# Performance work log

Measured on AMD Instinct MI355X. Metric: run time of the kernel, lower is better.

Reference implementation:

```python
import jax, jax.numpy as jnp
import numpy as np

EPS = 1e-6
DIM, HEADS, HEAD_DIM, FFN = 1024, 16, 64, 4096
B, S = 2, 2048


def layer_norm(x, g, b):
    m = jnp.mean(x, axis=-1, keepdims=True)
    v = jnp.mean(jnp.square(x - m), axis=-1, keepdims=True)
    return (x - m) * jax.lax.rsqrt(v + EPS) * g + b


def apply_rope(x, cos, sin):
    # x: (b, h, s, d); cos/sin: (s, d) broadcast over b, h
    x1, x2 = jnp.split(x, 2, axis=-1)
    rot = jnp.concatenate([-x2, x1], axis=-1)
    return x * cos + rot * sin


def setup_inputs() -> dict:
    key = jax.random.key(0)
    ks = jax.random.split(key, 24)
    sc_in = 1.0 / np.sqrt(DIM)
    sc_ffn = 1.0 / np.sqrt(FFN)
    inp = {
        "x": jax.random.normal(ks[0], (B, S, DIM), jnp.float32),
        "rope_cos": jax.random.uniform(ks[1], (S, HEAD_DIM), jnp.float32),
        "rope_sin": jax.random.uniform(ks[2], (S, HEAD_DIM), jnp.float32),
        "w_qkv": jax.random.normal(ks[3], (3 * DIM, DIM), jnp.float32) * sc_in,
        "b_qkv": jnp.zeros((3 * DIM,), jnp.float32),
        "w_out": jax.random.normal(ks[4], (DIM, DIM), jnp.float32) * sc_in,
        "b_out": jnp.zeros((DIM,), jnp.float32),
        "qn_g": jnp.ones((DIM,), jnp.float32),
        "qn_b": jnp.zeros((DIM,), jnp.float32),
        "kn_g": jnp.ones((DIM,), jnp.float32),
        "kn_b": jnp.zeros((DIM,), jnp.float32),
        "ln1_g": jnp.ones((DIM,), jnp.float32),
        "ln1_b": jnp.zeros((DIM,), jnp.float32),
        "ln2_g": jnp.ones((DIM,), jnp.float32),
        "ln2_b": jnp.zeros((DIM,), jnp.float32),
        "w1": jax.random.normal(ks[5], (FFN, DIM), jnp.float32) * sc_in,
        "b1": jnp.zeros((FFN,), jnp.float32),
        "w2": jax.random.normal(ks[6], (DIM, FFN), jnp.float32) * sc_ffn,
        "b2": jnp.zeros((DIM,), jnp.float32),
        "w3": jax.random.normal(ks[7], (FFN, DIM), jnp.float32) * sc_in,
        "b3": jnp.zeros((FFN,), jnp.float32),
    }
    return inp


def reference(x, rope_cos, rope_sin, w_qkv, b_qkv, w_out, b_out,
              qn_g, qn_b, kn_g, kn_b, ln1_g, ln1_b, ln2_g, ln2_b,
              w1, b1, w2, b2, w3, b3):
    bs, s, d = x.shape
    # --- pre-norm self-attention ---
    h = layer_norm(x, ln1_g, ln1_b)
    qkv = h @ w_qkv.T + b_qkv                      # (b, s, 3d)
    q, k, v = jnp.split(qkv, 3, axis=-1)
    q = layer_norm(q, qn_g, qn_b)                  # QK-norm over full dim
    k = layer_norm(k, kn_g, kn_b)
    # (b, s, d) -> (b, h, s, hd)
    q = q.reshape(bs, s, HEADS, HEAD_DIM).transpose(0, 2, 1, 3)
    k = k.reshape(bs, s, HEADS, HEAD_DIM).transpose(0, 2, 1, 3)
    v = v.reshape(bs, s, HEADS, HEAD_DIM).transpose(0, 2, 1, 3)
    q = apply_rope(q, rope_cos, rope_sin)
    k = apply_rope(k, rope_cos, rope_sin)
    scale = 1.0 / np.sqrt(HEAD_DIM)
    scores = jnp.einsum('bhqd,bhkd->bhqk', q, k) * scale
    probs = jax.nn.softmax(scores, axis=-1)
    attn = jnp.einsum('bhqk,bhkd->bhqd', probs, v)
    attn = attn.transpose(0, 2, 1, 3).reshape(bs, s, d)
    x = x + (attn @ w_out.T + b_out)
    # --- pre-norm SwiGLU FFN ---
    h2 = layer_norm(x, ln2_g, ln2_b)
    ffn = (jax.nn.silu(h2 @ w1.T + b1) * (h2 @ w3.T + b3)) @ w2.T + b2
    return x + ffn
```

## Files before the change

### kernel.cpp

```cpp
#include <hip/hip_runtime.h>
#include <hip/hip_bf16.h>


typedef __bf16 bf16_t;
typedef bf16_t bf16x8 __attribute__((ext_vector_type(8)));
typedef bf16_t bf16x4 __attribute__((ext_vector_type(4)));
typedef float  f32x4  __attribute__((ext_vector_type(4)));
typedef float  f32x16 __attribute__((ext_vector_type(16)));

#define DIM   1024
#define HEADS 16
#define HD    64
#define FFND  4096
#define NB    2
#define SEQ   2048
#define NTOK  (NB * SEQ)

#define GLOAD16(gp, lp) __builtin_amdgcn_global_load_lds( \
    (const __attribute__((address_space(1))) void*)(gp),  \
    (__attribute__((address_space(3))) void*)(lp), 16, 0, 0)

#define CVTPK(lo, hi_) ({ unsigned r_;                                        \
  asm("v_cvt_pk_bf16_f32 %0, %1, %2" : "=v"(r_) : "v"(lo), "v"(hi_)); r_; })
#define PLSWAP(a, b) asm("v_permlane32_swap_b32 %0, %1" : "+v"(a), "+v"(b))

#define F2B_S0 786432
#define F2B_S1 262144
#define F2B_S2 1048576
#define F2B_S3 1048576
#define F2B_S4 1048576
#define F2B_C1 (F2B_S0)
#define F2B_C2 (F2B_C1 + F2B_S1)
#define F2B_C3 (F2B_C2 + F2B_S2)
#define F2B_C4 (F2B_C3 + F2B_S3)
#define F2B_N  (F2B_C4 + F2B_S4)

__global__ void f2bf_all_kernel(const float* __restrict__ s0, const float* __restrict__ s1,
                                const float* __restrict__ s2, const float* __restrict__ s3,
                                const float* __restrict__ s4,
                                bf16_t* __restrict__ d0, bf16_t* __restrict__ d1,
                                bf16_t* __restrict__ d2, bf16_t* __restrict__ d3,
                                bf16_t* __restrict__ d4) {
  int idx = blockIdx.x * blockDim.x + threadIdx.x;
  int stride = gridDim.x * blockDim.x;
  for (; idx < F2B_N; idx += stride) {
    const float* src; bf16_t* dst; int i;
    if (idx < F2B_C1)      { src = s0; dst = d0; i = idx; }
    else if (idx < F2B_C2) { src = s1; dst = d1; i = idx - F2B_C1; }
    else if (idx < F2B_C3) { src = s2; dst = d2; i = idx - F2B_C2; }
    else if (idx < F2B_C4) { src = s3; dst = d3; i = idx - F2B_C3; }
    else                   { src = s4; dst = d4; i = idx - F2B_C4; }
    float4 v = reinterpret_cast<const float4*>(src)[i];
    bf16x4 o;
    o[0] = (bf16_t)v.x; o[1] = (bf16_t)v.y; o[2] = (bf16_t)v.z; o[3] = (bf16_t)v.w;
    reinterpret_cast<bf16x4*>(dst)[i] = o;
  }
}

__global__ __launch_bounds__(256) void ln_kernel(
    const float* __restrict__ x, const float* __restrict__ g,
    const float* __restrict__ b, bf16_t* __restrict__ out) {
  int t = blockIdx.x;
  int i = threadIdx.x;
  float4 v = reinterpret_cast<const float4*>(x + (size_t)t * DIM)[i];
  float s  = v.x + v.y + v.z + v.w;
  float s2 = v.x * v.x + v.y * v.y + v.z * v.z + v.w * v.w;
#pragma unroll
  for (int off = 32; off > 0; off >>= 1) {
    s  += __shfl_down(s, off, 64);
    s2 += __shfl_down(s2, off, 64);
  }
  __shared__ float red[2][4];
  int wid = i >> 6, lane = i & 63;
  if (lane == 0) { red[0][wid] = s; red[1][wid] = s2; }
  __syncthreads();
  float S  = red[0][0] + red[0][1] + red[0][2] + red[0][3];
  float S2 = red[1][0] + red[1][1] + red[1][2] + red[1][3];
  float mean = S * (1.0f / DIM);
  float var  = S2 * (1.0f / DIM) - mean * mean;
  float r = rsqrtf(var + 1e-6f);
  float vv[4] = {v.x, v.y, v.z, v.w};
  bf16x4 o;
#pragma unroll
  for (int j = 0; j < 4; ++j) {
    int d = i * 4 + j;
    o[j] = (bf16_t)((vv[j] - mean) * r * g[d] + b[d]);
  }
  *reinterpret_cast<bf16x4*>(out + (size_t)t * DIM + i * 4) = o;
}

template <int OUT_MODE>
__global__ __launch_bounds__(512, 2) void gemm256(
    const bf16_t* __restrict__ A, const bf16_t* __restrict__ B,
    const float* __restrict__ bias, const bf16_t* __restrict__ comp,
    void* __restrict__ Cout, int M, int N, int Kfull, int Klen) {
  __shared__ __align__(16) bf16_t Al[2][256][64];
  __shared__ __align__(16) bf16_t Bl[2][256][64];
  const int nTn = N >> 8;
  const int nwg = gridDim.x;
  const int bid = blockIdx.x;
  const int swz = ((nwg & 7) == 0) ? ((bid & 7) * (nwg >> 3) + (bid >> 3)) : bid;
  const int bm = swz / nTn, bn = swz % nTn;
  const int k0base = blockIdx.z * Klen;
  const int NT = Klen >> 6;
  const int tid = threadIdx.x, wid = tid >> 6, lane = tid & 63;
  const int wm = wid >> 2, wn = wid & 3;
  const int lr = lane & 15, lg = lane >> 4;
  const int strow = wid * 8 + (lane >> 3);
  const int stg   = ((lane & 7) ^ ((lane >> 3) & 7)) << 3;
  const bf16_t* Abase = A + (size_t)(bm * 256 + strow) * Kfull + k0base + stg;
  const bf16_t* Bbase = B + (size_t)(bn * 256 + strow) * Kfull + k0base + stg;

#define STAGE_A(buf, half, c, t)                                              \
  GLOAD16(Abase + (size_t)((half) * 128 + (c) * 64) * Kfull + (t) * 64,       \
          &Al[buf][(half) * 128 + (c) * 64 + wid * 8][0])
#define STAGE_B(buf, half, c, t)                                              \
  GLOAD16(Bbase + (size_t)((half) * 128 + (c) * 64) * Kfull + (t) * 64,       \
          &Bl[buf][(half) * 128 + (c) * 64 + wid * 8][0])

  f32x4 acc[8][4] = {};
  STAGE_A(0, 0, 0, 0); STAGE_A(0, 0, 1, 0); STAGE_A(0, 1, 0, 0); STAGE_A(0, 1, 1, 0);
  STAGE_B(0, 0, 0, 0); STAGE_B(0, 0, 1, 0); STAGE_B(0, 1, 0, 0); STAGE_B(0, 1, 1, 0);

  for (int t = 0; t < NT; ++t) {
    const int cur = t & 1, nxt = cur ^ 1;
    const bool pf = (t + 1 < NT);
    if (pf) {
      STAGE_A(nxt, 0, 0, t + 1); STAGE_A(nxt, 0, 1, t + 1);
      STAGE_A(nxt, 1, 0, t + 1); STAGE_A(nxt, 1, 1, t + 1);
      asm volatile("s_waitcnt vmcnt(4)");
    } else {
      asm volatile("s_waitcnt vmcnt(0)");
    }
    __builtin_amdgcn_sched_barrier(0);
    __builtin_amdgcn_s_barrier();
    __builtin_amdgcn_sched_barrier(0);
    bf16x8 bfr[4][2], af[2][2];
#pragma unroll
    for (int nf = 0; nf < 4; ++nf)
#pragma unroll
      for (int ks = 0; ks < 2; ++ks) {
        const int row = wn * 64 + nf * 16 + lr;
        const int g = ((ks * 4 + lg) ^ (lane & 7)) << 3;
        bfr[nf][ks] = *reinterpret_cast<const bf16x8*>(&Bl[cur][row][g]);
      }
#pragma unroll
    for (int i = 0; i < 2; ++i)
#pragma unroll
      for (int ks = 0; ks < 2; ++ks) {
        const int row = wm * 128 + i * 16 + lr;
        const int g = ((ks * 4 + lg) ^ (lane & 7)) << 3;
        af[i][ks] = *reinterpret_cast<const bf16x8*>(&Al[cur][row][g]);
      }
    asm volatile("s_waitcnt lgkmcnt(0)");
    __builtin_amdgcn_sched_barrier(0);
    __builtin_amdgcn_s_setprio(1);
#pragma unroll
    for (int i = 0; i < 2; ++i)
#pragma unroll
      for (int nf = 0; nf < 4; ++nf)
#pragma unroll
        for (int ks = 0; ks < 2; ++ks)
          acc[i][nf] = __builtin_amdgcn_mfma_f32_16x16x32_bf16(af[i][ks], bfr[nf][ks], acc[i][nf], 0, 0, 0);
    __builtin_amdgcn_s_setprio(0);
    __builtin_amdgcn_s_barrier();
#pragma unroll
    for (int p = 1; p < 4; ++p) {
#pragma unroll
      for (int i = 0; i < 2; ++i)
#pragma unroll
        for (int ks = 0; ks < 2; ++ks) {
          const int row = wm * 128 + (p * 2 + i) * 16 + lr;
          const int g = ((ks * 4 + lg) ^ (lane & 7)) << 3;
          af[i][ks] = *reinterpret_cast<const bf16x8*>(&Al[cur][row][g]);
        }
      if (p == 1 && pf) {
        STAGE_B(nxt, 0, 0, t + 1); STAGE_B(nxt, 0, 1, t + 1);
        STAGE_B(nxt, 1, 0, t + 1); STAGE_B(nxt, 1, 1, t + 1);
      }
      __builtin_amdgcn_s_barrier();
      asm volatile("s_waitcnt lgkmcnt(0)");
      __builtin_amdgcn_sched_barrier(0);
      __builtin_amdgcn_s_setprio(1);
#pragma unroll
      for (int i = 0; i < 2; ++i)
#pragma unroll
        for (int nf = 0; nf < 4; ++nf)
#pragma unroll
          for (int ks = 0; ks < 2; ++ks)
            acc[p * 2 + i][nf] = __builtin_amdgcn_mfma_f32_16x16x32_bf16(af[i][ks], bfr[nf][ks], acc[p * 2 + i][nf], 0, 0, 0);
      __builtin_amdgcn_s_setprio(0);
      __builtin_amdgcn_s_barrier();
    }
  }
#undef STAGE_A
#undef STAGE_B
  const int r0 = lg * 4;
#pragma unroll
  for (int mf = 0; mf < 8; ++mf) {
#pragma unroll
    for (int r = 0; r < 4; ++r) {
      const int row = bm * 256 + wm * 128 + mf * 16 + r0 + r;
#pragma unroll
      for (int nf = 0; nf < 4; ++nf) {
        const int col = bn * 256 + wn * 64 + nf * 16 + lr;
        float v = acc[mf][nf][r];
        if (OUT_MODE == 1) {
          v += bias[col];
          reinterpret_cast<bf16_t*>(Cout)[(size_t)row * N + col] = (bf16_t)v;
        } else if (OUT_MODE == 2) {
          float* P = reinterpret_cast<float*>(Cout) + (size_t)blockIdx.z * M * N;
          P[(size_t)row * N + col] = v;
        } else {
          v += bias[col];
          float c1 = (float)comp[(size_t)row * N + col];
          float sg = c1 / (1.0f + __expf(-c1));
          reinterpret_cast<bf16_t*>(Cout)[(size_t)row * N + col] = (bf16_t)(sg * v);
        }
      }
    }
  }
}

__global__ void combine_kernel(const float* __restrict__ part,
                               const float* __restrict__ bias,
                               const float* __restrict__ res,
                               float* __restrict__ out, int n4) {
  const int slice = NTOK * DIM / 4;
  int i = blockIdx.x * blockDim.x + threadIdx.x;
  int stride = gridDim.x * blockDim.x;
  const float4* p = reinterpret_cast<const float4*>(part);
  const float4* r4 = reinterpret_cast<const float4*>(res);
  const float4* b4 = reinterpret_cast<const float4*>(bias);
  float4* o4 = reinterpret_cast<float4*>(out);
  for (; i < n4; i += stride) {
    float4 a = p[i], b = p[i + slice], c = p[i + 2 * slice], d = p[i + 3 * slice];
    float4 rr = r4[i];
    float4 bb = b4[i & 255];
    float4 o;
    o.x = a.x + b.x + c.x + d.x + bb.x + rr.x;
    o.y = a.y + b.y + c.y + d.y + bb.y + rr.y;
    o.z = a.z + b.z + c.z + d.z + bb.z + rr.z;
    o.w = a.w + b.w + c.w + d.w + bb.w + rr.w;
    o4[i] = o;
  }
}

template <int OUT_BF16, int HAS_RES>
__global__ __launch_bounds__(256) void gemm_bt(
    const bf16_t* __restrict__ A, const bf16_t* __restrict__ B,
    const float* __restrict__ bias, const float* __restrict__ res,
    void* __restrict__ Cout, int M, int N, int K) {
  __shared__ bf16_t As[128][32];
  __shared__ bf16_t Bs[128][32];
  const int nTn = N >> 7;
  const int bm = blockIdx.x / nTn;
  const int bn = blockIdx.x % nTn;
  const int tid  = threadIdx.x;
  const int wid  = tid >> 6;
  const int lane = tid & 63;
  const int wm = (wid >> 1) * 64, wn = (wid & 1) * 64;
  const int lr = lane & 15;
  const int gq = lane >> 4;
  const int sr = lane >> 2;
  const int sg = lane & 3;
  const int cS = ((sg ^ ((sr >> 1) & 3)) << 3);
  const int swg = ((gq ^ ((lr >> 1) & 3)) << 3);
  f32x4 acc[4][4] = {};
  const bf16_t* Ag0 = A + (size_t)(bm * 128 + wid * 16 + sr) * K + cS;
  const bf16_t* Ag1 = Ag0 + (size_t)64 * K;
  const bf16_t* Bg0 = B + (size_t)(bn * 128 + wid * 16 + sr) * K + cS;
  const bf16_t* Bg1 = Bg0 + (size_t)64 * K;
  bf16_t* ldsA0 = &As[wid * 16][0];
  bf16_t* ldsA1 = &As[64 + wid * 16][0];
  bf16_t* ldsB0 = &Bs[wid * 16][0];
  bf16_t* ldsB1 = &Bs[64 + wid * 16][0];
  for (int k0 = 0; k0 < K; k0 += 32) {
    __syncthreads();
    GLOAD16(Ag0 + k0, ldsA0);
    GLOAD16(Ag1 + k0, ldsA1);
    GLOAD16(Bg0 + k0, ldsB0);
    GLOAD16(Bg1 + k0, ldsB1);
    __syncthreads();
    bf16x8 af[4], bfr[4];
#pragma unroll
    for (int mi = 0; mi < 4; ++mi)
      af[mi] = *reinterpret_cast<const bf16x8*>(&As[wm + mi * 16 + lr][swg]);
#pragma unroll
    for (int ni = 0; ni < 4; ++ni)
      bfr[ni] = *reinterpret_cast<const bf16x8*>(&Bs[wn + ni * 16 + lr][swg]);
#pragma unroll
    for (int mi = 0; mi < 4; ++mi)
#pragma unroll
      for (int ni = 0; ni < 4; ++ni)
        acc[mi][ni] = __builtin_amdgcn_mfma_f32_16x16x32_bf16(af[mi], bfr[ni], acc[mi][ni], 0, 0, 0);
  }
  const int r0 = (lane >> 4) * 4;
#pragma unroll
  for (int mi = 0; mi < 4; ++mi) {
#pragma unroll
    for (int r = 0; r < 4; ++r) {
      int row = bm * 128 + wm + mi * 16 + r0 + r;
#pragma unroll
      for (int ni = 0; ni < 4; ++ni) {
        int col = bn * 128 + wn + ni * 16 + lr;
        float v = acc[mi][ni][r] + bias[col];
        if (HAS_RES) v += res[(size_t)row * N + col];
        if (OUT_BF16)
          reinterpret_cast<bf16_t*>(Cout)[(size_t)row * N + col] = (bf16_t)v;
        else
          reinterpret_cast<float*>(Cout)[(size_t)row * N + col] = v;
      }
    }
  }
}

__global__ __launch_bounds__(256) void qknorm_rope_kernel(
    const bf16_t* __restrict__ qkv,
    const float* __restrict__ qg, const float* __restrict__ qb,
    const float* __restrict__ kg, const float* __restrict__ kb,
    const float* __restrict__ rc, const float* __restrict__ rs,
    bf16_t* __restrict__ q_r, bf16_t* __restrict__ k_r) {
  int t = blockIdx.x;
  int b = t >> 11, s = t & 2047;
  const bf16_t* p = qkv + (size_t)t * 3072;
  int i = threadIdx.x;
  bf16x4 qv = *reinterpret_cast<const bf16x4*>(p + i * 4);
  bf16x4 kv = *reinterpret_cast<const bf16x4*>(p + 1024 + i * 4);
  float q4[4], k4[4];
  float sq = 0.f, sq2 = 0.f, sk = 0.f, sk2 = 0.f;
#pragma unroll
  for (int j = 0; j < 4; ++j) {
    q4[j] = (float)qv[j]; k4[j] = (float)kv[j];
    sq += q4[j]; sq2 += q4[j] * q4[j];
    sk += k4[j]; sk2 += k4[j] * k4[j];
  }
#pragma unroll
  for (int off = 32; off > 0; off >>= 1) {
    sq  += __shfl_down(sq, off, 64);
    sq2 += __shfl_down(sq2, off, 64);
    sk  += __shfl_down(sk, off, 64);
    sk2 += __shfl_down(sk2, off, 64);
  }
  __shared__ float red[4][4];
  int wid = i >> 6, lane = i & 63;
  if (lane == 0) { red[0][wid] = sq; red[1][wid] = sq2; red[2][wid] = sk; red[3][wid] = sk2; }
  __syncthreads();
  float Sq  = red[0][0] + red[0][1] + red[0][2] + red[0][3];
  float Sq2 = red[1][0] + red[1][1] + red[1][2] + red[1][3];
  float Sk  = red[2][0] + red[2][1] + red[2][2] + red[2][3];
  float Sk2 = red[3][0] + red[3][1] + red[3][2] + red[3][3];
  float mq = Sq * (1.0f / DIM);
  float vq = Sq2 * (1.0f / DIM) - mq * mq;
  float rq = rsqrtf(vq + 1e-6f);
  float mk = Sk * (1.0f / DIM);
  float vk = Sk2 * (1.0f / DIM) - mk * mk;
  float rk = rsqrtf(vk + 1e-6f);
  const float QS = 0.18033688011f;
#pragma unroll
  for (int j = 0; j < 4; ++j) {
    int d = i * 4 + j, h = d >> 6, hd = d & 63, dp = d ^ 32;
    float c  = rc[s * HD + hd];
    float sn = rs[s * HD + hd];
    float qn  = (q4[j] - mq) * rq * qg[d] + qb[d];
    float qpn = ((float)p[dp] - mq) * rq * qg[dp] + qb[dp];
    float qo  = qn * c + ((hd < 32) ? -qpn : qpn) * sn;
    float kn  = (k4[j] - mk) * rk * kg[d] + kb[d];
    float kpn = ((float)p[1024 + dp] - mk) * rk * kg[dp] + kb[dp];
    float ko  = kn * c + ((hd < 32) ? -kpn : kpn) * sn;
    size_t oi = ((size_t)(b * HEADS + h) * SEQ + s) * HD + hd;
    q_r[oi] = (bf16_t)(qo * QS);
    k_r[oi] = (bf16_t)ko;
  }
}

__global__ __launch_bounds__(256) void vtrans_kernel(
    const bf16_t* __restrict__ qkv, bf16_t* __restrict__ v_t) {
  __shared__ bf16_t T[64][72];
  const int st = blockIdx.x;
  const int bh = blockIdx.y;
  const int b = bh >> 4, h = bh & 15;
  const int tid = threadIdx.x;
  const int r = tid >> 2, c = (tid & 3) * 8;
  const bf16_t* src = qkv + (size_t)(b * SEQ + st * 64 + r) * 3072 + 2048 + h * 64;
  *reinterpret_cast<bf16x8*>(&T[r][c])      = *reinterpret_cast<const bf16x8*>(src + c);
  *reinterpret_cast<bf16x8*>(&T[r][c + 32]) = *reinterpret_cast<const bf16x8*>(src + c + 32);
  __syncthreads();
  bf16x8 o0, o1;
#pragma unroll
  for (int j = 0; j < 8; ++j) { o0[j] = T[c + j][r]; o1[j] = T[c + 32 + j][r]; }
  bf16_t* dst = v_t + ((size_t)bh * 64 + r) * SEQ + st * 64;
  *reinterpret_cast<bf16x8*>(dst + c)      = o0;
  *reinterpret_cast<bf16x8*>(dst + c + 32) = o1;
}

__global__ __launch_bounds__(256) void attn_kernel(
    const bf16_t* __restrict__ q_r, const bf16_t* __restrict__ k_r,
    const bf16_t* __restrict__ v_t, bf16_t* __restrict__ attn_out) {
  __shared__ __align__(16) bf16_t Ks[2][4096];
  __shared__ __align__(16) bf16_t Vs[2][4096];
  const int bid = blockIdx.x;
  const int hh = bid & 31;
  const int qt = bid >> 5;
  const int bidx = hh >> 4, h = hh & 15;
  const bf16_t* Qp = q_r + (size_t)hh * SEQ * HD;
  const bf16_t* Kp = k_r + (size_t)hh * SEQ * HD;
  const bf16_t* Vp = v_t + (size_t)hh * HD * SEQ;
  const int tid = threadIdx.x, wid = tid >> 6, lane = tid & 63;
  const int lq = lane & 31, hi = lane >> 5;
  const int qglob = qt * 128 + wid * 32 + lq;
  bf16x8 qf[4];
#pragma unroll
  for (int kdt = 0; kdt < 4; ++kdt)
    qf[kdt] = *reinterpret_cast<const bf16x8*>(Qp + (size_t)qglob * HD + kdt * 16 + hi * 8);
  union { unsigned u[4]; bf16x8 v; } ones_;
  ones_.u[0] = ones_.u[1] = ones_.u[2] = ones_.u[3] = 0x3F803F80u;
  f32x16 o0 = {}, o1 = {}, lacc = {};
  const int sA = tid, sB = tid + 256;
  const int rA = sA >> 3, gA = (sA & 7) ^ (rA & 7);
  const int rB = sB >> 3, gB = (sB & 7) ^ (rB & 7);
  const int koffA = rA * HD + gA * 8,  koffB = rB * HD + gB * 8;
  const int voffA = rA * SEQ + gA * 8, voffB = rB * SEQ + gB * 8;
  const int ldsA = wid * 512, ldsB = 2048 + wid * 512;
  const int sw = lq & 7;
  GLOAD16(Kp + koffA, &Ks[0][ldsA]);
  GLOAD16(Kp + koffB, &Ks[0][ldsB]);
  GLOAD16(Vp + voffA, &Vs[0][ldsA]);
  GLOAD16(Vp + voffB, &Vs[0][ldsB]);
  __syncthreads();
  for (int kt = 0; kt < SEQ / 64; ++kt) {
    const int cur = kt & 1, nxt = cur ^ 1;
    if (kt + 1 < SEQ / 64) {
      GLOAD16(Kp + (kt + 1) * (64 * HD) + koffA, &Ks[nxt][ldsA]);
      GLOAD16(Kp + (kt + 1) * (64 * HD) + koffB, &Ks[nxt][ldsB]);
      GLOAD16(Vp + (kt + 1) * 64 + voffA, &Vs[nxt][ldsA]);
      GLOAD16(Vp + (kt + 1) * 64 + voffB, &Vs[nxt][ldsB]);
    }
    f32x16 s0 = {}, s1 = {};
#pragma unroll
    for (int kdt = 0; kdt < 4; ++kdt) {
      const int g = ((kdt * 2 + hi) ^ sw) * 8;
      bf16x8 kf0 = *reinterpret_cast<const bf16x8*>(&Ks[cur][lq * HD + g]);
      bf16x8 kf1 = *reinterpret_cast<const bf16x8*>(&Ks[cur][(lq + 32) * HD + g]);
      s0 = __builtin_amdgcn_mfma_f32_32x32x16_bf16(kf0, qf[kdt], s0, 0, 0, 0);
      s1 = __builtin_amdgcn_mfma_f32_32x32x16_bf16(kf1, qf[kdt], s1, 0, 0, 0);
    }
#pragma unroll
    for (int i = 0; i < 16; ++i) s0[i] = __builtin_amdgcn_exp2f(s0[i]);
#pragma unroll
    for (int i = 0; i < 16; ++i) s1[i] = __builtin_amdgcn_exp2f(s1[i]);
#pragma unroll
    for (int tt = 0; tt < 2; ++tt) {
      const f32x16& p = tt ? s1 : s0;
#pragma unroll
      for (int ks = 0; ks < 2; ++ks) {
        unsigned a, b, c, d;
        if (ks == 0) {
          a = CVTPK(p[0], p[1]); b = CVTPK(p[4], p[5]);
          c = CVTPK(p[2], p[3]); d = CVTPK(p[6], p[7]);
        } else {
          a = CVTPK(p[8], p[9]);  b = CVTPK(p[12], p[13]);
          c = CVTPK(p[10], p[11]); d = CVTPK(p[14], p[15]);
        }
        PLSWAP(a, b); PLSWAP(c, d);
        union { unsigned u[4]; bf16x8 v; } pf;
        pf.u[0] = a; pf.u[1] = c; pf.u[2] = b; pf.u[3] = d;
        const int gv = ((tt * 4 + ks * 2 + hi) ^ sw) * 8;
        bf16x8 vf0 = *reinterpret_cast<const bf16x8*>(&Vs[cur][lq * HD + gv]);
        bf16x8 vf1 = *reinterpret_cast<const bf16x8*>(&Vs[cur][(lq + 32) * HD + gv]);
        o0 = __builtin_amdgcn_mfma_f32_32x32x16_bf16(vf0, pf.v, o0, 0, 0, 0);
        o1 = __builtin_amdgcn_mfma_f32_32x32x16_bf16(vf1, pf.v, o1, 0, 0, 0);
        lacc = __builtin_amdgcn_mfma_f32_32x32x16_bf16(ones_.v, pf.v, lacc, 0, 0, 0);
      }
    }
    __syncthreads();
  }
  float inv = 1.0f / lacc[0];
  bf16_t* orow = attn_out + ((size_t)(bidx * SEQ + qglob)) * DIM + h * 64;
#pragma unroll
  for (int g = 0; g < 4; ++g) {
    bf16x4 w0, w1;
#pragma unroll
    for (int j = 0; j < 4; ++j) {
      w0[j] = (bf16_t)(o0[g * 4 + j] * inv);
      w1[j] = (bf16_t)(o1[g * 4 + j] * inv);
    }
    *reinterpret_cast<bf16x4*>(orow + g * 8 + 4 * hi)      = w0;
    *reinterpret_cast<bf16x4*>(orow + 32 + g * 8 + 4 * hi) = w1;
  }
}

extern "C" void kernel_launch(void* const* d_in, const int* in_sizes, int n_in,
                              void* d_out, int out_size, void* d_ws, size_t ws_size,
                              hipStream_t stream) {
  const float* x        = (const float*)d_in[0];
  const float* rope_cos = (const float*)d_in[1];
  const float* rope_sin = (const float*)d_in[2];
  const float* w_qkv    = (const float*)d_in[3];
  const float* b_qkv    = (const float*)d_in[4];
  const float* w_out    = (const float*)d_in[5];
  const float* b_out    = (const float*)d_in[6];
  const float* qn_g     = (const float*)d_in[7];
  const float* qn_b     = (const float*)d_in[8];
  const float* kn_g     = (const float*)d_in[9];
  const float* kn_b     = (const float*)d_in[10];
  const float* ln1_g    = (const float*)d_in[11];
  const float* ln1_b    = (const float*)d_in[12];
  const float* ln2_g    = (const float*)d_in[13];
  const float* ln2_b    = (const float*)d_in[14];
  const float* w1       = (const float*)d_in[15];
  const float* b1       = (const float*)d_in[16];
  const float* w2       = (const float*)d_in[17];
  const float* b2       = (const float*)d_in[18];
  const float* w3       = (const float*)d_in[19];
  const float* b3       = (const float*)d_in[20];

  const size_t OFF_WQKV = 0;
  const size_t OFF_WOUT = 6291456;
  const size_t OFF_W1   = 8388608;
  const size_t OFF_W2   = 16777216;
  const size_t OFF_W3   = 25165824;
  const size_t OFF_H1   = 33554432;
  const size_t OFF_QKV  = 41943040;
  const size_t OFF_QR   = 67108864;
  const size_t OFF_KR   = 75497472;
  const size_t OFF_VT   = 83886080;
  const size_t OFF_ATT  = 92274688;
  const size_t OFF_X2   = 100663296;
  const size_t OFF_H2   = 117440512;
  const size_t OFF_A1   = 33554432;
  const size_t OFF_A3   = 67108864;
  const size_t OFF_PART = 125829120;
  const size_t NEEDED   = 125829120;
  const size_t NEED_SPLIT = OFF_PART + 67108864;
  if (ws_size < NEEDED) return;
  const bool use_split = (ws_size >= NEED_SPLIT);

  char* ws = (char*)d_ws;
  bf16_t* wqkv_bf = (bf16_t*)(ws + OFF_WQKV);
  bf16_t* wout_bf = (bf16_t*)(ws + OFF_WOUT);
  bf16_t* w1_bf   = (bf16_t*)(ws + OFF_W1);
  bf16_t* w2_bf   = (bf16_t*)(ws + OFF_W2);
  bf16_t* w3_bf   = (bf16_t*)(ws + OFF_W3);
  bf16_t* h1      = (bf16_t*)(ws + OFF_H1);
  bf16_t* qkv     = (bf16_t*)(ws + OFF_QKV);
  bf16_t* q_r     = (bf16_t*)(ws + OFF_QR);
  bf16_t* k_r     = (bf16_t*)(ws + OFF_KR);
  bf16_t* v_t     = (bf16_t*)(ws + OFF_VT);
  bf16_t* att     = (bf16_t*)(ws + OFF_ATT);
  float*  x2      = (float*)(ws + OFF_X2);
  bf16_t* h2      = (bf16_t*)(ws + OFF_H2);
  bf16_t* a1      = (bf16_t*)(ws + OFF_A1);
  bf16_t* a3      = (bf16_t*)(ws + OFF_A3);
  float*  part    = (float*)(ws + OFF_PART);
  float*  out     = (float*)d_out;

  f2bf_all_kernel<<<2048, 256, 0, stream>>>(w_qkv, w_out, w1, w2, w3,
                                            wqkv_bf, wout_bf, w1_bf, w2_bf, w3_bf);
  ln_kernel<<<NTOK, 256, 0, stream>>>(x, ln1_g, ln1_b, h1);
  gemm256<1><<<dim3(192, 1, 1), 512, 0, stream>>>(h1, wqkv_bf, b_qkv, nullptr, qkv,
                                                  NTOK, 3072, DIM, DIM);
  qknorm_rope_kernel<<<NTOK, 256, 0, stream>>>(qkv, qn_g, qn_b, kn_g, kn_b,
                                               rope_cos, rope_sin, q_r, k_r);
  vtrans_kernel<<<dim3(SEQ / 64, NB * HEADS), 256, 0, stream>>>(qkv, v_t);
  attn_kernel<<<512, 256, 0, stream>>>(q_r, k_r, v_t, att);
  gemm_bt<0, 1><<<32 * 8, 256, 0, stream>>>(att, wout_bf, b_out, x, x2, NTOK, DIM, DIM);
  ln_kernel<<<NTOK, 256, 0, stream>>>(x2, ln2_g, ln2_b, h2);
  gemm256<1><<<dim3(256, 1, 1), 512, 0, stream>>>(h2, w1_bf, b1, nullptr, a1,
                                                  NTOK, FFND, DIM, DIM);
  gemm256<3><<<dim3(256, 1, 1), 512, 0, stream>>>(h2, w3_bf, b3, a1, a3,
                                                  NTOK, FFND, DIM, DIM);
  if (use_split) {
    gemm256<2><<<dim3(64, 1, 4), 512, 0, stream>>>(a3, w2_bf, nullptr, nullptr, part,
                                                   NTOK, DIM, FFND, FFND / 4);
    combine_kernel<<<2048, 256, 0, stream>>>(part, b2, x2, out, NTOK * DIM / 4);
  } else {
    gemm_bt<0, 1><<<32 * 8, 256, 0, stream>>>(a3, w2_bf, b2, x2, out, NTOK, DIM, FFND);
  }
}
```

Baseline: 331.1 us.

## Double per-wave query tile in attention and compute row sums with VALU

Each wave now handles 64 query rows (two 32-row groups) rather than 32, so every K/V fragment read from LDS feeds twice as many MFMAs, and the grid drops from 512 to 256 blocks. The softmax denominator is now summed with VALU adds plus a cross-half shuffle, replacing the extra ones-vector MFMA. The LDS layout also changes from an XOR-swizzled row layout to a column-group-major layout. The cost is higher register pressure and only 256 blocks, which may leave some of the GPU's compute units underused.

Result: slower. 344.1 us (+3.9%).

```diff
diff --git a/kernel.cpp b/kernel.cpp
--- a/kernel.cpp
+++ b/kernel.cpp
@@ -408,85 +408,117 @@
   const bf16_t* Vp = v_t + (size_t)hh * HD * SEQ;
   const int tid = threadIdx.x, wid = tid >> 6, lane = tid & 63;
   const int lq = lane & 31, hi = lane >> 5;
-  const int qglob = qt * 128 + wid * 32 + lq;
-  bf16x8 qf[4];
-#pragma unroll
-  for (int kdt = 0; kdt < 4; ++kdt)
-    qf[kdt] = *reinterpret_cast<const bf16x8*>(Qp + (size_t)qglob * HD + kdt * 16 + hi * 8);
-  union { unsigned u[4]; bf16x8 v; } ones_;
-  ones_.u[0] = ones_.u[1] = ones_.u[2] = ones_.u[3] = 0x3F803F80u;
-  f32x16 o0 = {}, o1 = {}, lacc = {};
-  const int sA = tid, sB = tid + 256;
-  const int rA = sA >> 3, gA = (sA & 7) ^ (rA & 7);
-  const int rB = sB >> 3, gB = (sB & 7) ^ (rB & 7);
-  const int koffA = rA * HD + gA * 8,  koffB = rB * HD + gB * 8;
-  const int voffA = rA * SEQ + gA * 8, voffB = rB * SEQ + gB * 8;
-  const int ldsA = wid * 512, ldsB = 2048 + wid * 512;
-  const int sw = lq & 7;
-  GLOAD16(Kp + koffA, &Ks[0][ldsA]);
-  GLOAD16(Kp + koffB, &Ks[0][ldsB]);
-  GLOAD16(Vp + voffA, &Vs[0][ldsA]);
-  GLOAD16(Vp + voffB, &Vs[0][ldsB]);
+  const int qA = qt * 256 + wid * 64 + lq;
+  const int qB = qA + 32;
+  bf16x8 qfA[4], qfB[4];
+#pragma unroll
+  for (int kdt = 0; kdt < 4; ++kdt) {
+    qfA[kdt] = *reinterpret_cast<const bf16x8*>(Qp + (size_t)qA * HD + kdt * 16 + hi * 8);
+    qfB[kdt] = *reinterpret_cast<const bf16x8*>(Qp + (size_t)qB * HD + kdt * 16 + hi * 8);
+  }
+  f32x16 oA0 = {}, oA1 = {}, oB0 = {}, oB1 = {};
+  float lA = 0.f, lB = 0.f;
+  const int kSrcA = lane * HD + wid * 8;
+  const int kSrcB = lane * HD + (wid + 4) * 8;
+  const int vSrcA = lane * SEQ + wid * 8;
+  const int vSrcB = lane * SEQ + (wid + 4) * 8;
+  const int ldsA = wid * 512;
+  const int ldsB = 2048 + wid * 512;
+  GLOAD16(Kp + kSrcA, &Ks[0][ldsA]);
+  GLOAD16(Kp + kSrcB, &Ks[0][ldsB]);
+  GLOAD16(Vp + vSrcA, &Vs[0][ldsA]);
+  GLOAD16(Vp + vSrcB, &Vs[0][ldsB]);
   __syncthreads();
   for (int kt = 0; kt < SEQ / 64; ++kt) {
     const int cur = kt & 1, nxt = cur ^ 1;
     if (kt + 1 < SEQ / 64) {
-      GLOAD16(Kp + (kt + 1) * (64 * HD) + koffA, &Ks[nxt][ldsA]);
-      GLOAD16(Kp + (kt + 1) * (64 * HD) + koffB, &Ks[nxt][ldsB]);
-      GLOAD16(Vp + (kt + 1) * 64 + voffA, &Vs[nxt][ldsA]);
-      GLOAD16(Vp + (kt + 1) * 64 + voffB, &Vs[nxt][ldsB]);
-    }
-    f32x16 s0 = {}, s1 = {};
+      GLOAD16(Kp + (kt + 1) * (64 * HD) + kSrcA, &Ks[nxt][ldsA]);
+      GLOAD16(Kp + (kt + 1) * (64 * HD) + kSrcB, &Ks[nxt][ldsB]);
+      GLOAD16(Vp + (kt + 1) * 64 + vSrcA, &Vs[nxt][ldsA]);
+      GLOAD16(Vp + (kt + 1) * 64 + vSrcB, &Vs[nxt][ldsB]);
+    }
+    f32x16 sA0 = {}, sA1 = {}, sB0 = {}, sB1 = {};
 #pragma unroll
     for (int kdt = 0; kdt < 4; ++kdt) {
-      const int g = ((kdt * 2 + hi) ^ sw) * 8;
-      bf16x8 kf0 = *reinterpret_cast<const bf16x8*>(&Ks[cur][lq * HD + g]);
-      bf16x8 kf1 = *reinterpret_cast<const bf16x8*>(&Ks[cur][(lq + 32) * HD + g]);
-      s0 = __builtin_amdgcn_mfma_f32_32x32x16_bf16(kf0, qf[kdt], s0, 0, 0, 0);
-      s1 = __builtin_amdgcn_mfma_f32_32x32x16_bf16(kf1, qf[kdt], s1, 0, 0, 0);
-    }
-#pragma unroll
-    for (int i = 0; i < 16; ++i) s0[i] = __builtin_amdgcn_exp2f(s0[i]);
-#pragma unroll
-    for (int i = 0; i < 16; ++i) s1[i] = __builtin_amdgcn_exp2f(s1[i]);
+      const int goff = (kdt * 2 + hi) * 512;
+      bf16x8 kf0 = *reinterpret_cast<const bf16x8*>(&Ks[cur][goff + lq * 8]);
+      bf16x8 kf1 = *reinterpret_cast<const bf16x8*>(&Ks[cur][goff + (lq + 32) * 8]);
+      sA0 = __builtin_amdgcn_mfma_f32_32x32x16_bf16(kf0, qfA[kdt], sA0, 0, 0, 0);
+      sA1 = __builtin_amdgcn_mfma_f32_32x32x16_bf16(kf1, qfA[kdt], sA1, 0, 0, 0);
+      sB0 = __builtin_amdgcn_mfma_f32_32x32x16_bf16(kf0, qfB[kdt], sB0, 0, 0, 0);
+      sB1 = __builtin_amdgcn_mfma_f32_32x32x16_bf16(kf1, qfB[kdt], sB1, 0, 0, 0);
+    }
+#pragma unroll
+    for (int i = 0; i < 16; ++i) sA0[i] = __builtin_amdgcn_exp2f(sA0[i]);
+#pragma unroll
+    for (int i = 0; i < 16; ++i) sA1[i] = __builtin_amdgcn_exp2f(sA1[i]);
+#pragma unroll
+    for (int i = 0; i < 16; ++i) sB0[i] = __builtin_amdgcn_exp2f(sB0[i]);
+#pragma unroll
+    for (int i = 0; i < 16; ++i) sB1[i] = __builtin_amdgcn_exp2f(sB1[i]);
+    {
+      f32x16 t = sA0 + sA1;
+      float a = ((t[0] + t[8]) + (t[4] + t[12])) + ((t[2] + t[10]) + (t[6] + t[14]));
+      float b = ((t[1] + t[9]) + (t[5] + t[13])) + ((t[3] + t[11]) + (t[7] + t[15]));
+      lA += a + b;
+      f32x16 u = sB0 + sB1;
+      float c = ((u[0] + u[8]) + (u[4] + u[12])) + ((u[2] + u[10]) + (u[6] + u[14]));
+      float d = ((u[1] + u[9]) + (u[5] + u[13])) + ((u[3] + u[11]) + (u[7] + u[15]));
+      lB += c + d;
+    }
 #pragma unroll
     for (int tt = 0; tt < 2; ++tt) {
-      const f32x16& p = tt ? s1 : s0;
 #pragma unroll
       for (int ks = 0; ks < 2; ++ks) {
-        unsigned a, b, c, d;
+        const f32x16& pA = tt ? sA1 : sA0;
+        const f32x16& pB = tt ? sB1 : sB0;
+        unsigned a0, b0, c0, d0, a1, b1, c1, d1;
         if (ks == 0) {
-          a = CVTPK(p[0], p[1]); b = CVTPK(p[4], p[5]);
-          c = CVTPK(p[2], p[3]); d = CVTPK(p[6], p[7]);
+          a0 = CVTPK(pA[0], pA[1]); b0 = CVTPK(pA[4], pA[5]);
+          c0 = CVTPK(pA[2], pA[3]); d0 = CVTPK(pA[6], pA[7]);
+          a1 = CVTPK(pB[0], pB[1]); b1 = CVTPK(pB[4], pB[5]);
+          c1 = CVTPK(pB[2], pB[3]); d1 = CVTPK(pB[6], pB[7]);
         } else {
-          a = CVTPK(p[8], p[9]);  b = CVTPK(p[12], p[13]);
-          c = CVTPK(p[10], p[11]); d = CVTPK(p[14], p[15]);
+          a0 = CVTPK(pA[8], pA[9]);   b0 = CVTPK(pA[12], pA[13]);
+          c0 = CVTPK(pA[10], pA[11]); d0 = CVTPK(pA[14], pA[15]);
+          a1 = CVTPK(pB[8], pB[9]);   b1 = CVTPK(pB[12], pB[13]);
+          c1 = CVTPK(pB[10], pB[11]); d1 = CVTPK(pB[14], pB[15]);
         }
-        PLSWAP(a, b); PLSWAP(c, d);
-        union { unsigned u[4]; bf16x8 v; } pf;
-        pf.u[0] = a; pf.u[1] = c; pf.u[2] = b; pf.u[3] = d;
-        const int gv = ((tt * 4 + ks * 2 + hi) ^ sw) * 8;
-        bf16x8 vf0 = *reinterpret_cast<const bf16x8*>(&Vs[cur][lq * HD + gv]);
-        bf16x8 vf1 = *reinterpret_cast<const bf16x8*>(&Vs[cur][(lq + 32) * HD + gv]);
-        o0 = __builtin_amdgcn_mfma_f32_32x32x16_bf16(vf0, pf.v, o0, 0, 0, 0);
-        o1 = __builtin_amdgcn_mfma_f32_32x32x16_bf16(vf1, pf.v, o1, 0, 0, 0);
-        lacc = __builtin_amdgcn_mfma_f32_32x32x16_bf16(ones_.v, pf.v, lacc, 0, 0, 0);
+        PLSWAP(a0, b0); PLSWAP(c0, d0); PLSWAP(a1, b1); PLSWAP(c1, d1);
+        union { unsigned u[4]; bf16x8 v; } pfA, pfB;
+        pfA.u[0] = a0; pfA.u[1] = c0; pfA.u[2] = b0; pfA.u[3] = d0;
+        pfB.u[0] = a1; pfB.u[1] = c1; pfB.u[2] = b1; pfB.u[3] = d1;
+        const int gv = (tt * 4 + ks * 2 + hi) * 512;
+        bf16x8 vf0 = *reinterpret_cast<const bf16x8*>(&Vs[cur][gv + lq * 8]);
+        bf16x8 vf1 = *reinterpret_cast<const bf16x8*>(&Vs[cur][gv + (lq + 32) * 8]);
+        oA0 = __builtin_amdgcn_mfma_f32_32x32x16_bf16(vf0, pfA.v, oA0, 0, 0, 0);
+        oA1 = __builtin_amdgcn_mfma_f32_32x32x16_bf16(vf1, pfA.v, oA1, 0, 0, 0);
+        oB0 = __builtin_amdgcn_mfma_f32_32x32x16_bf16(vf0, pfB.v, oB0, 0, 0, 0);
+        oB1 = __builtin_amdgcn_mfma_f32_32x32x16_bf16(vf1, pfB.v, oB1, 0, 0, 0);
       }
     }
     __syncthreads();
   }
-  float inv = 1.0f / lacc[0];
-  bf16_t* orow = attn_out + ((size_t)(bidx * SEQ + qglob)) * DIM + h * 64;
+  lA += __shfl_xor(lA, 32, 64);
+  lB += __shfl_xor(lB, 32, 64);
+  float invA = 1.0f / lA;
+  float invB = 1.0f / lB;
+  bf16_t* orowA = attn_out + ((size_t)(bidx * SEQ + qA)) * DIM + h * 64;
+  bf16_t* orowB = attn_out + ((size_t)(bidx * SEQ + qB)) * DIM + h * 64;
 #pragma unroll
   for (int g = 0; g < 4; ++g) {
-    bf16x4 w0, w1;
+    bf16x4 wA0, wA1, wB0, wB1;
 #pragma unroll
     for (int j = 0; j < 4; ++j) {
-      w0[j] = (bf16_t)(o0[g * 4 + j] * inv);
-      w1[j] = (bf16_t)(o1[g * 4 + j] * inv);
-    }
-    *reinterpret_cast<bf16x4*>(orow + g * 8 + 4 * hi)      = w0;
-    *reinterpret_cast<bf16x4*>(orow + 32 + g * 8 + 4 * hi) = w1;
+      wA0[j] = (bf16_t)(oA0[g * 4 + j] * invA);
+      wA1[j] = (bf16_t)(oA1[g * 4 + j] * invA);
+      wB0[j] = (bf16_t)(oB0[g * 4 + j] * invB);
+      wB1[j] = (bf16_t)(oB1[g * 4 + j] * invB);
+    }
+    *reinterpret_cast<bf16x4*>(orowA + g * 8 + 4 * hi)      = wA0;
+    *reinterpret_cast<bf16x4*>(orowA + 32 + g * 8 + 4 * hi) = wA1;
+    *reinterpret_cast<bf16x4*>(orowB + g * 8 + 4 * hi)      = wB0;
+    *reinterpret_cast<bf16x4*>(orowB + 32 + g * 8 + 4 * hi) = wB1;
   }
 }
 
@@ -563,7 +595,7 @@
   qknorm_rope_kernel<<<NTOK, 256, 0, stream>>>(qkv, qn_g, qn_b, kn_g, kn_b,
                                                rope_cos, rope_sin, q_r, k_r);
   vtrans_kernel<<<dim3(SEQ / 64, NB * HEADS), 256, 0, stream>>>(qkv, v_t);
-  attn_kernel<<<512, 256, 0, stream>>>(q_r, k_r, v_t, att);
+  attn_kernel<<<256, 256, 0, stream>>>(q_r, k_r, v_t, att);
   gemm_bt<0, 1><<<32 * 8, 256, 0, stream>>>(att, wout_bf, b_out, x, x2, NTOK, DIM, DIM);
   ln_kernel<<<NTOK, 256, 0, stream>>>(x2, ln2_g, ln2_b, h2);
   gemm256<1><<<dim3(256, 1, 1), 512, 0, stream>>>(h2, w1_bf, b1, nullptr, a1,
```
